# Optimization experiments

Measured on AMD Instinct MI355X. Metric: run time of the kernel, lower is better.

Reference implementation:

```python
import jax, jax.numpy as jnp
import numpy as np

EMB, HID, VOC, NLAYERS, TLEN = 256, 512, 32000, 2, 64
SRC_LEN, BS = 128, 64
DEC_HID = 2 * HID  # decoder hidden = hidden_dim * 2


def _p(key, shape, scale=0.05):
    return jax.random.normal(key, shape, dtype=jnp.float32) * scale


def setup_inputs() -> dict:
    key = jax.random.key(0)
    ks = jax.random.split(key, 24)
    d = {}
    d["sentences"] = jax.random.randint(ks[0], (SRC_LEN, BS), 0, VOC)
    d["targets"] = jax.random.randint(ks[1], (TLEN, BS), 0, VOC)
    d["emb"] = _p(ks[2], (VOC, EMB))
    # encoder: bidirectional, 2 layers; gate order i,f,g,o (PyTorch)
    d["enc0_Wih"] = _p(ks[3], (2, 4 * HID, EMB))
    d["enc0_Whh"] = _p(ks[4], (2, 4 * HID, HID))
    d["enc0_bih"] = _p(ks[5], (2, 4 * HID))
    d["enc0_bhh"] = _p(ks[6], (2, 4 * HID))
    d["enc1_Wih"] = _p(ks[7], (2, 4 * HID, 2 * HID))
    d["enc1_Whh"] = _p(ks[8], (2, 4 * HID, HID))
    d["enc1_bih"] = _p(ks[9], (2, 4 * HID))
    d["enc1_bhh"] = _p(ks[10], (2, 4 * HID))
    # decoder: unidirectional, 2 layers, hidden DEC_HID
    d["dec0_Wih"] = _p(ks[11], (4 * DEC_HID, EMB))
    d["dec0_Whh"] = _p(ks[12], (4 * DEC_HID, DEC_HID))
    d["dec0_bih"] = _p(ks[13], (4 * DEC_HID,))
    d["dec0_bhh"] = _p(ks[14], (4 * DEC_HID,))
    d["dec1_Wih"] = _p(ks[15], (4 * DEC_HID, DEC_HID))
    d["dec1_Whh"] = _p(ks[16], (4 * DEC_HID, DEC_HID))
    d["dec1_bih"] = _p(ks[17], (4 * DEC_HID,))
    d["dec1_bhh"] = _p(ks[18], (4 * DEC_HID,))
    d["W_out"] = _p(ks[19], (VOC, DEC_HID))
    d["b_out"] = _p(ks[20], (VOC,))
    return d


def lstm_scan(x, h0, c0, Wih, Whh, bih, bhh, reverse=False):
    # x: (T,B,In). Precompute input projection for the whole sequence.
    xw = jnp.einsum('tbi,gi->tbg', x, Wih) + bih  # (T,B,4H)

    def step(carry, g_in):
        h, c = carry
        g = g_in + h @ Whh.T + bhh
        i, f, gg, o = jnp.split(g, 4, axis=-1)
        c = jax.nn.sigmoid(f) * c + jax.nn.sigmoid(i) * jnp.tanh(gg)
        h = jax.nn.sigmoid(o) * jnp.tanh(c)
        return (h, c), h

    (hT, cT), ys = jax.lax.scan(step, (h0, c0), xw, reverse=reverse)
    return ys, hT, cT


def _forward(sentences, targets, emb,
             enc0_Wih, enc0_Whh, enc0_bih, enc0_bhh,
             enc1_Wih, enc1_Whh, enc1_bih, enc1_bhh,
             dec0_Wih, dec0_Whh, dec0_bih, dec0_bhh,
             dec1_Wih, dec1_Whh, dec1_bih, dec1_bhh,
             W_out, b_out):
    bs = sentences.shape[1]
    x = emb[sentences]  # (S,B,E)
    z = jnp.zeros((bs, HID), jnp.float32)
    enc_layers = ((enc0_Wih, enc0_Whh, enc0_bih, enc0_bhh),
                  (enc1_Wih, enc1_Whh, enc1_bih, enc1_bhh))
    hs, cs = [], []
    for Wih, Whh, bih, bhh in enc_layers:
        yf, hf, cf = lstm_scan(x, z, z, Wih[0], Whh[0], bih[0], bhh[0])
        yb, hb, cb = lstm_scan(x, z, z, Wih[1], Whh[1], bih[1], bhh[1], reverse=True)
        x = jnp.concatenate([yf, yb], axis=-1)  # (S,B,2H)
        hs.append(jnp.concatenate([hf, hb], axis=-1))  # _reshape_hidden concat
        cs.append(jnp.concatenate([cf, cb], axis=-1))
    # teacher forcing: decoder inputs are last source token, then targets[:-1]
    dec_tokens = jnp.concatenate([sentences[-1:], targets[:-1]], axis=0)  # (T,B)
    y = emb[dec_tokens]  # (T,B,E); dropout is identity in eval mode
    dec_layers = ((dec0_Wih, dec0_Whh, dec0_bih, dec0_bhh),
                  (dec1_Wih, dec1_Whh, dec1_bih, dec1_bhh))
    for l, (Wih, Whh, bih, bhh) in enumerate(dec_layers):
        y, _, _ = lstm_scan(y, hs[l], cs[l], Wih, Whh, bih, bhh)
    logits = jnp.einsum('tbh,vh->tbv', y, W_out) + b_out  # (T,B,V)
    return jax.nn.log_softmax(logits, axis=-1)


def reference(sentences, targets, emb,
              enc0_Wih, enc0_Whh, enc0_bih, enc0_bhh,
              enc1_Wih, enc1_Whh, enc1_bih, enc1_bhh,
              dec0_Wih, dec0_Whh, dec0_bih, dec0_bhh,
              dec1_Wih, dec1_Whh, dec1_bih, dec1_bhh,
              W_out, b_out):
    return _forward(sentences, targets, emb,
                    enc0_Wih, enc0_Whh, enc0_bih, enc0_bhh,
                    enc1_Wih, enc1_Whh, enc1_bih, enc1_bhh,
                    dec0_Wih, dec0_Whh, dec0_bih, dec0_bhh,
                    dec1_Wih, dec1_Whh, dec1_bih, dec1_bhh,
                    W_out, b_out)
```

## Files before the change

kernel.cpp:

```cpp
#include <hip/hip_runtime.h>

#define S_LEN 128
#define T_LEN 64
#define BSZ   64
#define EMBD  256
#define HID_  512
#define DHID_ 1024
#define VOC_  32000
#define HSTR  1024

typedef float  f4_t  __attribute__((ext_vector_type(4)));
typedef float  f32x4 __attribute__((ext_vector_type(4)));
typedef short  s16x8 __attribute__((ext_vector_type(8)));
typedef __bf16 bf16x8 __attribute__((ext_vector_type(8)));
typedef unsigned short u16x4 __attribute__((ext_vector_type(4)));
typedef int    i32x2 __attribute__((ext_vector_type(2)));

#define WS_XWA  0ull
#define WS_XWB  (WS_XWA + 16777216ull)
#define WS_CS   (WS_XWB + 16777216ull)
#define WS_BAR  (WS_CS  + 131072ull)
#define WS_BF   (WS_BAR + 32768ull)
#define U_X0B   0ull
#define U_HE0   (U_X0B + 2097152ull)
#define U_HE1   (U_HE0 + 8388608ull)
#define U_HD0   (U_HE1 + 8388608ull)
#define U_HD1   (U_HD0 + 4194304ull)
#define U_HSB   (U_HD1 + 4194304ull)
#define U_E0W   (U_HSB + 131072ull)
#define U_E1W   (U_E0W + 1048576ull)
#define U_D0W   (U_E1W + 4194304ull)
#define U_D1W   (U_D0W + 1048576ull)

__device__ __forceinline__ unsigned short f2bf(float x) {
    unsigned u = __builtin_bit_cast(unsigned, x);
    return (unsigned short)((u + 0x7fffu + ((u >> 16) & 1u)) >> 16);
}

__device__ __forceinline__ f4_t sc_load4(const void* p) {
    f4_t v;
    asm volatile("global_load_dwordx4 %0, %1, off sc0 sc1" : "=v"(v) : "v"(p));
    return v;
}
__device__ __forceinline__ int sc_load1(const int* p) {
    int v;
    asm volatile("global_load_dword %0, %1, off sc0 sc1\n\ts_waitcnt vmcnt(0)"
                 : "=v"(v) : "v"(p) : "memory");
    return v;
}
__device__ __forceinline__ void sc_store_int(int* p, int v) {
    asm volatile("global_store_dword %0, %1, off sc0 sc1" :: "v"(p), "v"(v) : "memory");
}
__device__ __forceinline__ void sc_store8(void* p, i32x2 v) {
    asm volatile("global_store_dwordx2 %0, %1, off sc0 sc1" :: "v"(p), "v"(v) : "memory");
}
__device__ __forceinline__ float g_load1(const float* p) {
    float v;
    asm volatile("global_load_dword %0, %1, off" : "=v"(v) : "v"(p));
    return v;
}
__device__ __forceinline__ void wait_vm0() {
    asm volatile("s_waitcnt vmcnt(0)" ::: "memory");
}
__device__ __forceinline__ void wait_vm8() {
    asm volatile("s_waitcnt vmcnt(8)" ::: "memory");
}

__device__ __forceinline__ void gload_lds16(const void* g, void* l) {
    __builtin_amdgcn_global_load_lds(
        (const __attribute__((address_space(1))) void*)g,
        (__attribute__((address_space(3))) void*)l, 16, 0, 0);
}

__device__ __forceinline__ float sigmoidf_(float x) { return 1.f / (1.f + expf(-x)); }

__global__ __launch_bounds__(256) void f2b_kernel(
    const float* __restrict__ in, unsigned short* __restrict__ out, int n4)
{
    const int stride = gridDim.x * 256;
    for (int i = blockIdx.x * 256 + threadIdx.x; i < n4; i += stride) {
        const float4 v = reinterpret_cast<const float4*>(in)[i];
        u16x4 o = { f2bf(v.x), f2bf(v.y), f2bf(v.z), f2bf(v.w) };
        reinterpret_cast<u16x4*>(out)[i] = o;
    }
}

__global__ __launch_bounds__(64) void embed_src_kernel(
    const int* __restrict__ toks, const float* __restrict__ emb,
    unsigned short* __restrict__ out)
{
    const int i = blockIdx.x;
    const int tok = toks[i];
    const float4 v = reinterpret_cast<const float4*>(emb + (size_t)tok * EMBD)[threadIdx.x];
    u16x4 o = { f2bf(v.x), f2bf(v.y), f2bf(v.z), f2bf(v.w) };
    reinterpret_cast<u16x4*>(out + (size_t)i * EMBD)[threadIdx.x] = o;
}

__global__ __launch_bounds__(64) void embed_dec_kernel(
    const int* __restrict__ sent, const int* __restrict__ targ,
    const float* __restrict__ emb, unsigned short* __restrict__ out)
{
    const int i = blockIdx.x;
    const int t = i >> 6, b = i & 63;
    const int tok = (t == 0) ? sent[(S_LEN - 1) * BSZ + b] : targ[(t - 1) * BSZ + b];
    const float4 v = reinterpret_cast<const float4*>(emb + (size_t)tok * EMBD)[threadIdx.x];
    u16x4 o = { f2bf(v.x), f2bf(v.y), f2bf(v.z), f2bf(v.w) };
    reinterpret_cast<u16x4*>(out + (size_t)i * EMBD)[threadIdx.x] = o;
}

__global__ __launch_bounds__(256) void gemm_bf16_kernel(
    const unsigned short* __restrict__ A, const unsigned short* __restrict__ B,
    const float* __restrict__ b1, const float* __restrict__ b2,
    float* __restrict__ C, int M, int N, int K, int nTN, int tmode)
{
    __shared__ __align__(16) unsigned short As[128 * 64];
    __shared__ __align__(16) unsigned short Bs[128 * 64];

    const int tid  = threadIdx.x;
    const int lane = tid & 63;
    const int wv   = tid >> 6;
    const int wm   = wv >> 1, wn = wv & 1;

    const int nwg = gridDim.x;
    const int q = nwg >> 3, r = nwg & 7;
    const int xcd = blockIdx.x & 7, io = blockIdx.x >> 3;
    const int wg = (xcd < r ? xcd * (q + 1) : r * (q + 1) + (xcd - r) * q) + io;
    const int bm = (wg / nTN) * 128;
    const int bn = (wg % nTN) * 128;

    f32x4 acc[4][4];
#pragma unroll
    for (int i = 0; i < 4; ++i)
#pragma unroll
        for (int j = 0; j < 4; ++j) acc[i][j] = (f32x4)0.f;

    const int lin_base = wv * 1024 + lane * 16;

    for (int k0 = 0; k0 < K; k0 += 64) {
        __syncthreads();
#pragma unroll
        for (int qc = 0; qc < 4; ++qc) {
            const int lin = qc * 4096 + lin_base;
            const int row = lin >> 7;
            const int c   = (lin >> 4) & 7;
            const int sc  = c ^ (row & 7);
            const size_t gofs  = (size_t)(bm + row) * K + k0 + sc * 8;
            const size_t gofsB = (size_t)(bn + row) * K + k0 + sc * 8;
            char* ldst  = (char*)As + qc * 4096 + wv * 1024;
            char* ldstB = (char*)Bs + qc * 4096 + wv * 1024;
            gload_lds16(A + gofs, ldst);
            gload_lds16(B + gofsB, ldstB);
        }
        asm volatile("s_waitcnt vmcnt(0)" ::: "memory");
        __syncthreads();
#pragma unroll
        for (int ks = 0; ks < 2; ++ks) {
            bf16x8 af[4], bfv[4];
            const int ca = ks * 4 + (lane >> 4);
#pragma unroll
            for (int f = 0; f < 4; ++f) {
                const int ra = wm * 64 + f * 16 + (lane & 15);
                af[f] = __builtin_bit_cast(bf16x8,
                    *(const s16x8*)((const char*)As + ra * 128 + ((ca ^ (ra & 7)) << 4)));
                const int rb = wn * 64 + f * 16 + (lane & 15);
                bfv[f] = __builtin_bit_cast(bf16x8,
                    *(const s16x8*)((const char*)Bs + rb * 128 + ((ca ^ (rb & 7)) << 4)));
            }
#pragma unroll
            for (int i = 0; i < 4; ++i)
#pragma unroll
                for (int j = 0; j < 4; ++j)
                    acc[i][j] = __builtin_amdgcn_mfma_f32_16x16x32_bf16(
                        af[i], bfv[j], acc[i][j], 0, 0, 0);
        }
    }

    const int col0 = bn + wn * 64 + (lane & 15);
    if (tmode == 0) {
        const int row0 = bm + wm * 64 + ((lane >> 4) << 2);
#pragma unroll
        for (int i = 0; i < 4; ++i) {
#pragma unroll
            for (int j = 0; j < 4; ++j) {
                const int col = col0 + j * 16;
                float bias = b1[col];
                if (b2) bias += b2[col];
#pragma unroll
                for (int rg = 0; rg < 4; ++rg)
                    C[(size_t)(row0 + i * 16 + rg) * N + col] = acc[i][j][rg] + bias;
            }
        }
    } else {
        const int tblk = (bm >> 6) + wm;
        const int rb = (lane >> 4) << 2;
#pragma unroll
        for (int i = 0; i < 4; ++i) {
#pragma unroll
            for (int j = 0; j < 4; ++j) {
                const int col = col0 + j * 16;
                float bias = b1[col];
                if (b2) bias += b2[col];
                float4 v = { acc[i][j][0] + bias, acc[i][j][1] + bias,
                             acc[i][j][2] + bias, acc[i][j][3] + bias };
                *reinterpret_cast<float4*>(&C[((size_t)tblk * N + col) * 64 + rb + i * 16]) = v;
            }
        }
    }
}

template<int H_T>
__global__ __launch_bounds__(256, 1) void lstm_mfma_scan(
    const float* __restrict__ xw0, const float* __restrict__ xw1,
    const float* __restrict__ Whh0, const float* __restrict__ Whh1,
    const unsigned short* __restrict__ h0b, const float* __restrict__ c0,
    unsigned short* __restrict__ hist,
    unsigned short* __restrict__ hsb, float* __restrict__ csd,
    int T, int ndir, int rev_mask, int* bar)
{
    constexpr int KST = H_T / 32;
    constexpr int CH  = H_T / 8;
    constexpr int NB  = CH / 32;

    __shared__ __align__(16) unsigned short h_lds[64 * H_T];
    __shared__ float pre[64][17];
    __shared__ __align__(8) unsigned short hpack[64][4];

    const int tid  = threadIdx.x;
    const int lane = tid & 63;
    const int w    = tid >> 6;
    const int bpd  = (ndir == 2) ? 128 : 256;
    const int dir  = blockIdx.x / bpd;
    const int blk  = blockIdx.x - dir * bpd;
    const int m0   = blk * 4;
    const int rev  = (rev_mask >> dir) & 1;
    const float* xw  = dir ? xw1  : xw0;
    const float* Whh = dir ? Whh1 : Whh0;
    const int dcol = dir * H_T;
    const int b = tid & 63;
    const int j = tid >> 6;

    int* myflag = bar + blockIdx.x * 32;
    const int* pollflag = bar + (dir * bpd + (tid < bpd ? tid : 0)) * 32;
    const bool polls = (tid < bpd);

    const int n  = lane & 15;
    const int kg = lane >> 4;
    const int wr = (n >> 2) * H_T + m0 + (n & 3);
    s16x8 wfr[KST];
#pragma unroll
    for (int ks = 0; ks < KST; ++ks) {
        const float* wp = Whh + (size_t)wr * H_T + ks * 32 + kg * 8;
        const float4 lo = *reinterpret_cast<const float4*>(wp);
        const float4 hi = *reinterpret_cast<const float4*>(wp + 4);
        s16x8 rr;
        rr[0] = (short)f2bf(lo.x); rr[1] = (short)f2bf(lo.y);
        rr[2] = (short)f2bf(lo.z); rr[3] = (short)f2bf(lo.w);
        rr[4] = (short)f2bf(hi.x); rr[5] = (short)f2bf(hi.y);
        rr[6] = (short)f2bf(hi.z); rr[7] = (short)f2bf(hi.w);
        wfr[ks] = rr;
    }

    float c  = c0 ? c0[(size_t)b * HSTR + dcol + m0 + j] : 0.f;
    float hn = 0.f;
    const int rA = w * 16 + n;
    const int rAx = rA & 7;

    for (int s = 0; s < T; ++s) {
        const int tt = rev ? (T - 1 - s) : s;

        const float* xb = xw + ((size_t)tt * (4 * H_T) + m0 + j) * 64 + b;
        float xg0 = g_load1(xb);
        float xg1 = g_load1(xb + (size_t)H_T * 64);
        float xg2 = g_load1(xb + (size_t)2 * H_T * 64);
        float xg3 = g_load1(xb + (size_t)3 * H_T * 64);

        if (s > 0) {
            int ok = polls ? 0 : 1;
            for (;;) {
                if (!ok) ok = (sc_load1(pollflag) >= s) ? 1 : 0;
                if (__syncthreads_and(ok)) break;
            }
        }

        const unsigned short* hb;
        size_t tofs;
        if (s == 0) { hb = h0b; tofs = 0; }
        else {
            const int tp = rev ? (tt + 1) : (tt - 1);
            hb = hist; tofs = (size_t)tp * (64 * 1024);
        }

        float p0 = 0.f, p1 = 0.f, p2 = 0.f, p3 = 0.f;
        if (hb) {
            f4_t bufA[8], bufB[8];
            auto issue = [&](f4_t (&bf)[8], int bt) {
#pragma unroll
                for (int jj = 0; jj < 8; ++jj) {
                    const int idx = (bt * 8 + jj) * 256 + tid;
                    const int rr_ = idx / CH, cc_ = idx % CH;
                    bf[jj] = sc_load4(hb + tofs + (size_t)rr_ * 1024 + dcol + cc_ * 8);
                }
            };
            auto writeb = [&](const f4_t (&bf)[8], int bt) {
#pragma unroll
                for (int jj = 0; jj < 8; ++jj) {
                    const int idx = (bt * 8 + jj) * 256 + tid;
                    const int rr_ = idx / CH, cc_ = idx % CH;
                    const int off = rr_ * (2 * H_T) + ((cc_ ^ (rr_ & 7)) << 4);
                    *(f4_t*)((char*)h_lds + off) = bf[jj];
                }
            };
            issue(bufA, 0);
            if (NB > 1) issue(bufB, 1);
#pragma unroll
            for (int bt = 0; bt < NB; ++bt) {
                if (bt + 1 < NB) wait_vm8(); else wait_vm0();
                if (bt & 1) writeb(bufB, bt); else writeb(bufA, bt);
                if (bt + 2 < NB) { if (bt & 1) issue(bufB, bt + 2); else issue(bufA, bt + 2); }
            }
            __syncthreads();

            f32x4 acc = {0.f, 0.f, 0.f, 0.f};
#pragma unroll
            for (int ks = 0; ks < KST; ++ks) {
                const int cc_ = ks * 4 + kg;
                const int off = rA * (2 * H_T) + ((cc_ ^ rAx) << 4);
                const bf16x8 a = __builtin_bit_cast(bf16x8,
                    *(const s16x8*)((const char*)h_lds + off));
                acc = __builtin_amdgcn_mfma_f32_16x16x32_bf16(
                    a, __builtin_bit_cast(bf16x8, wfr[ks]), acc, 0, 0, 0);
            }
            __syncthreads();
#pragma unroll
            for (int rg = 0; rg < 4; ++rg)
                pre[w * 16 + kg * 4 + rg][n] = acc[rg];
            __syncthreads();
            p0 = pre[b][0 + j]; p1 = pre[b][4 + j];
            p2 = pre[b][8 + j]; p3 = pre[b][12 + j];
        }

        asm volatile("s_waitcnt vmcnt(0)"
                     : "+v"(xg0), "+v"(xg1), "+v"(xg2), "+v"(xg3) :: "memory");

        const float ig = sigmoidf_(p0 + xg0);
        const float fg = sigmoidf_(p1 + xg1);
        const float gg = tanhf(p2 + xg2);
        const float og = sigmoidf_(p3 + xg3);
        c  = fg * c + ig * gg;
        hn = og * tanhf(c);

        hpack[b][j] = f2bf(hn);
        __syncthreads();
        if (tid < 64) {
            const i32x2 v2 = *reinterpret_cast<const i32x2*>(&hpack[tid][0]);
            sc_store8(hist + (size_t)tt * (64 * 1024) + (size_t)tid * 1024 + dcol + m0, v2);
        }
        wait_vm0();
        __syncthreads();
        if (s + 1 < T && tid == 0) sc_store_int(myflag, s + 1);
    }

    if (hsb) hsb[(size_t)b * 1024 + dcol + m0 + j] = f2bf(hn);
    if (csd) csd[(size_t)b * HSTR + dcol + m0 + j] = c;
}

__global__ __launch_bounds__(256) void logsoftmax_kernel(float* __restrict__ x, int n4)
{
    const int tid = threadIdx.x;
    float4* p = reinterpret_cast<float4*>(x + (size_t)blockIdx.x * (n4 * 4));
    float m = -3.0e38f, s = 0.f;
    for (int cc = tid; cc < n4; cc += 256) {
        const float4 v = p[cc];
        const float vv[4] = { v.x, v.y, v.z, v.w };
#pragma unroll
        for (int e = 0; e < 4; ++e) {
            const float z = vv[e];
            if (z > m) { s = s * expf(m - z) + 1.f; m = z; }
            else       { s += expf(z - m); }
        }
    }
    __shared__ float ms[256], ss[256];
    ms[tid] = m; ss[tid] = s;
    __syncthreads();
    for (int off = 128; off > 0; off >>= 1) {
        if (tid < off) {
            const float m2 = ms[tid + off], s2 = ss[tid + off];
            const float m1 = ms[tid],       s1 = ss[tid];
            const float M = fmaxf(m1, m2);
            ss[tid] = s1 * expf(m1 - M) + s2 * expf(m2 - M);
            ms[tid] = M;
        }
        __syncthreads();
    }
    const float ML = ms[0] + logf(ss[0]);
    for (int cc = tid; cc < n4; cc += 256) {
        float4 v = p[cc];
        v.x -= ML; v.y -= ML; v.z -= ML; v.w -= ML;
        p[cc] = v;
    }
}

extern "C" void kernel_launch(void* const* d_in, const int* in_sizes, int n_in,
                              void* d_out, int out_size, void* d_ws, size_t ws_size,
                              hipStream_t stream)
{
    const int*   sent  = (const int*)d_in[0];
    const int*   targ  = (const int*)d_in[1];
    const float* emb   = (const float*)d_in[2];
    const float* e0Wih = (const float*)d_in[3];
    const float* e0Whh = (const float*)d_in[4];
    const float* e0bih = (const float*)d_in[5];
    const float* e0bhh = (const float*)d_in[6];
    const float* e1Wih = (const float*)d_in[7];
    const float* e1Whh = (const float*)d_in[8];
    const float* e1bih = (const float*)d_in[9];
    const float* e1bhh = (const float*)d_in[10];
    const float* d0Wih = (const float*)d_in[11];
    const float* d0Whh = (const float*)d_in[12];
    const float* d0bih = (const float*)d_in[13];
    const float* d0bhh = (const float*)d_in[14];
    const float* d1Wih = (const float*)d_in[15];
    const float* d1Whh = (const float*)d_in[16];
    const float* d1bih = (const float*)d_in[17];
    const float* d1bhh = (const float*)d_in[18];
    const float* Wout  = (const float*)d_in[19];
    const float* bout  = (const float*)d_in[20];

    float* ws  = (float*)d_ws;
    float* xwA = ws + WS_XWA;
    float* xwB = ws + WS_XWB;
    float* cs  = ws + WS_CS;
    int*   bar = (int*)(ws + WS_BAR);
    unsigned short* ub    = (unsigned short*)(ws + WS_BF);
    unsigned short* x0b   = ub + U_X0B;
    unsigned short* h_e0  = ub + U_HE0;
    unsigned short* h_e1  = ub + U_HE1;
    unsigned short* h_d0  = ub + U_HD0;
    unsigned short* h_d1  = ub + U_HD1;
    unsigned short* hsb   = ub + U_HSB;
    unsigned short* e0Wb  = ub + U_E0W;
    unsigned short* e1Wb  = ub + U_E1W;
    unsigned short* d0Wb  = ub + U_D0W;
    unsigned short* d1Wb  = ub + U_D1W;
    unsigned short* Woutb = (unsigned short*)xwA;
    float* out = (float*)d_out;

    hipMemsetAsync(bar, 0, 4 * 8192 * sizeof(int), stream);

    f2b_kernel<<<256, 256, 0, stream>>>(e0Wih, e0Wb, 1048576 / 4);
    f2b_kernel<<<512, 256, 0, stream>>>(e1Wih, e1Wb, 4194304 / 4);
    f2b_kernel<<<256, 256, 0, stream>>>(d0Wih, d0Wb, 1048576 / 4);
    f2b_kernel<<<512, 256, 0, stream>>>(d1Wih, d1Wb, 4194304 / 4);

    embed_src_kernel<<<S_LEN * BSZ, 64, 0, stream>>>(sent, emb, x0b);
    gemm_bf16_kernel<<<64 * 16, 256, 0, stream>>>(x0b, e0Wb, e0bih, e0bhh, xwA,
                                                  S_LEN * BSZ, 2048, EMBD, 16, 1);
    gemm_bf16_kernel<<<64 * 16, 256, 0, stream>>>(x0b, e0Wb + 2048ull * 256,
                                                  e0bih + 2048, e0bhh + 2048, xwB,
                                                  S_LEN * BSZ, 2048, EMBD, 16, 1);
    lstm_mfma_scan<512><<<256, 256, 0, stream>>>(xwA, xwB, e0Whh, e0Whh + 2048ull * 512,
                                                 nullptr, nullptr, h_e0,
                                                 hsb, cs, S_LEN, 2, 2, bar);
    gemm_bf16_kernel<<<64 * 16, 256, 0, stream>>>(h_e0, e1Wb, e1bih, e1bhh, xwA,
                                                  S_LEN * BSZ, 2048, 2 * HID_, 16, 1);
    gemm_bf16_kernel<<<64 * 16, 256, 0, stream>>>(h_e0, e1Wb + 2048ull * 1024,
                                                  e1bih + 2048, e1bhh + 2048, xwB,
                                                  S_LEN * BSZ, 2048, 2 * HID_, 16, 1);
    lstm_mfma_scan<512><<<256, 256, 0, stream>>>(xwA, xwB, e1Whh, e1Whh + 2048ull * 512,
                                                 nullptr, nullptr, h_e1,
                                                 hsb + 65536, cs + 65536,
                                                 S_LEN, 2, 2, bar + 8192);
    embed_dec_kernel<<<T_LEN * BSZ, 64, 0, stream>>>(sent, targ, emb, x0b);
    gemm_bf16_kernel<<<32 * 32, 256, 0, stream>>>(x0b, d0Wb, d0bih, d0bhh, xwA,
                                                  T_LEN * BSZ, 4 * DHID_, EMBD, 32, 1);
    lstm_mfma_scan<1024><<<256, 256, 0, stream>>>(xwA, nullptr, d0Whh, nullptr,
                                                  hsb, cs, h_d0,
                                                  nullptr, nullptr, T_LEN, 1, 0,
                                                  bar + 2 * 8192);
    f2b_kernel<<<2048, 256, 0, stream>>>(Wout, Woutb, (VOC_ * DHID_) / 4);
    gemm_bf16_kernel<<<32 * 32, 256, 0, stream>>>(h_d0, d1Wb, d1bih, d1bhh, xwB,
                                                  T_LEN * BSZ, 4 * DHID_, DHID_, 32, 1);
    lstm_mfma_scan<1024><<<256, 256, 0, stream>>>(xwB, nullptr, d1Whh, nullptr,
                                                  hsb + 65536, cs + 65536, h_d1,
                                                  nullptr, nullptr, T_LEN, 1, 0,
                                                  bar + 3 * 8192);
    gemm_bf16_kernel<<<32 * 250, 256, 0, stream>>>(h_d1, Woutb, bout, nullptr, out,
                                                   T_LEN * BSZ, VOC_, DHID_, 250, 0);
    logsoftmax_kernel<<<T_LEN * BSZ, 256, 0, stream>>>(out, VOC_ / 4);
}
```

Baseline: 2.711 ms.

## Split LSTM scan by batch halves, keep Whh in LDS, store gate preactivations as bf16

The recurrent scan kernel is reorganized so each block handles 8 hidden cells for half the batch. This halves the per-step h history loaded into LDS and moves the recurrent weights from registers into LDS. The gate nonlinearities are computed in the MFMA lanes and combined via lane shuffles, which removes the pre-activation LDS round trip and two barriers per step. The input-projection GEMM now writes bf16 instead of fp32, halving xw traffic, and the next step's xw load is prefetched. This trades some precision in the gate pre-activations, and the barrier groups become per-batch-half sets of blocks.

```diff
diff --git a/kernel.cpp b/kernel.cpp
--- a/kernel.cpp
+++ b/kernel.cpp
@@ -16,25 +16,29 @@
 typedef unsigned short u16x4 __attribute__((ext_vector_type(4)));
 typedef int    i32x2 __attribute__((ext_vector_type(2)));
 
-#define WS_XWA  0ull
-#define WS_XWB  (WS_XWA + 16777216ull)
-#define WS_CS   (WS_XWB + 16777216ull)
-#define WS_BAR  (WS_CS  + 131072ull)
+#define WS_CS   0ull
+#define WS_BAR  (WS_CS + 131072ull)
 #define WS_BF   (WS_BAR + 32768ull)
 #define U_X0B   0ull
-#define U_HE0   (U_X0B + 2097152ull)
-#define U_HE1   (U_HE0 + 8388608ull)
-#define U_HD0   (U_HE1 + 8388608ull)
-#define U_HD1   (U_HD0 + 4194304ull)
-#define U_HSB   (U_HD1 + 4194304ull)
-#define U_E0W   (U_HSB + 131072ull)
-#define U_E1W   (U_E0W + 1048576ull)
-#define U_D0W   (U_E1W + 4194304ull)
-#define U_D1W   (U_D0W + 1048576ull)
+#define U_HE0   (U_X0B  + 2097152ull)
+#define U_HE1   (U_HE0  + 8388608ull)
+#define U_HD0   (U_HE1  + 8388608ull)
+#define U_HD1   (U_HD0  + 4194304ull)
+#define U_HSB   (U_HD1  + 4194304ull)
+#define U_E0W   (U_HSB  + 131072ull)
+#define U_E1W   (U_E0W  + 1048576ull)
+#define U_D0W   (U_E1W  + 4194304ull)
+#define U_D1W   (U_D0W  + 1048576ull)
+#define U_XWA   (U_D1W  + 4194304ull)
+#define U_XWB   (U_XWA  + 16777216ull)
+#define U_WOUT  (U_XWB  + 16777216ull)
 
 __device__ __forceinline__ unsigned short f2bf(float x) {
     unsigned u = __builtin_bit_cast(unsigned, x);
     return (unsigned short)((u + 0x7fffu + ((u >> 16) & 1u)) >> 16);
+}
+__device__ __forceinline__ float bf2f(unsigned u) {
+    return __builtin_bit_cast(float, u << 16);
 }
 
 __device__ __forceinline__ f4_t sc_load4(const void* p) {
@@ -51,12 +55,12 @@
 __device__ __forceinline__ void sc_store_int(int* p, int v) {
     asm volatile("global_store_dword %0, %1, off sc0 sc1" :: "v"(p), "v"(v) : "memory");
 }
-__device__ __forceinline__ void sc_store8(void* p, i32x2 v) {
-    asm volatile("global_store_dwordx2 %0, %1, off sc0 sc1" :: "v"(p), "v"(v) : "memory");
-}
-__device__ __forceinline__ float g_load1(const float* p) {
-    float v;
-    asm volatile("global_load_dword %0, %1, off" : "=v"(v) : "v"(p));
+__device__ __forceinline__ void sc_store_short(unsigned short* p, unsigned v) {
+    asm volatile("global_store_short %0, %1, off sc0 sc1" :: "v"(p), "v"(v) : "memory");
+}
+__device__ __forceinline__ i32x2 g_load8(const void* p) {
+    i32x2 v;
+    asm volatile("global_load_dwordx2 %0, %1, off" : "=v"(v) : "v"(p));
     return v;
 }
 __device__ __forceinline__ void wait_vm0() {
@@ -111,7 +115,7 @@
 __global__ __launch_bounds__(256) void gemm_bf16_kernel(
     const unsigned short* __restrict__ A, const unsigned short* __restrict__ B,
     const float* __restrict__ b1, const float* __restrict__ b2,
-    float* __restrict__ C, int M, int N, int K, int nTN, int tmode)
+    void* __restrict__ Cv, int M, int N, int K, int nTN, int tmode)
 {
     __shared__ __align__(16) unsigned short As[128 * 64];
     __shared__ __align__(16) unsigned short Bs[128 * 64];
@@ -177,6 +181,7 @@
 
     const int col0 = bn + wn * 64 + (lane & 15);
     if (tmode == 0) {
+        float* C = (float*)Cv;
         const int row0 = bm + wm * 64 + ((lane >> 4) << 2);
 #pragma unroll
         for (int i = 0; i < 4; ++i) {
@@ -191,6 +196,7 @@
             }
         }
     } else {
+        unsigned short* C = (unsigned short*)Cv;
         const int tblk = (bm >> 6) + wm;
         const int rb = (lane >> 4) << 2;
 #pragma unroll
@@ -200,9 +206,9 @@
                 const int col = col0 + j * 16;
                 float bias = b1[col];
                 if (b2) bias += b2[col];
-                float4 v = { acc[i][j][0] + bias, acc[i][j][1] + bias,
-                             acc[i][j][2] + bias, acc[i][j][3] + bias };
-                *reinterpret_cast<float4*>(&C[((size_t)tblk * N + col) * 64 + rb + i * 16]) = v;
+                u16x4 o = { f2bf(acc[i][j][0] + bias), f2bf(acc[i][j][1] + bias),
+                            f2bf(acc[i][j][2] + bias), f2bf(acc[i][j][3] + bias) };
+                *reinterpret_cast<u16x4*>(&C[((size_t)tblk * N + col) * 64 + rb + i * 16]) = o;
             }
         }
     }
@@ -210,7 +216,7 @@
 
 template<int H_T>
 __global__ __launch_bounds__(256, 1) void lstm_mfma_scan(
-    const float* __restrict__ xw0, const float* __restrict__ xw1,
+    const unsigned short* __restrict__ xw0, const unsigned short* __restrict__ xw1,
     const float* __restrict__ Whh0, const float* __restrict__ Whh1,
     const unsigned short* __restrict__ h0b, const float* __restrict__ c0,
     unsigned short* __restrict__ hist,
@@ -219,37 +225,44 @@
 {
     constexpr int KST = H_T / 32;
     constexpr int CH  = H_T / 8;
-    constexpr int NB  = CH / 32;
-
-    __shared__ __align__(16) unsigned short h_lds[64 * H_T];
-    __shared__ float pre[64][17];
-    __shared__ __align__(8) unsigned short hpack[64][4];
+    constexpr int CPT = CH / 8;
+    constexpr int NBH = CPT / 8;
+    constexpr int NCB = H_T / 8;
+
+    __shared__ __align__(16) unsigned short h_lds[32 * H_T];
+    __shared__ __align__(16) unsigned short w_lds[32 * H_T];
 
     const int tid  = threadIdx.x;
     const int lane = tid & 63;
     const int w    = tid >> 6;
-    const int bpd  = (ndir == 2) ? 128 : 256;
-    const int dir  = blockIdx.x / bpd;
-    const int blk  = blockIdx.x - dir * bpd;
-    const int m0   = blk * 4;
+    const int bq   = w & 1;
+    const int rh   = w >> 1;
+    const int n    = lane & 15;
+    const int kg   = lane >> 4;
+    const int g    = n >> 2;
+    const int cell = rh * 4 + (n & 3);
+
+    const int nbpd = 2 * NCB;
+    const int dir  = blockIdx.x / nbpd;
+    const int rem  = blockIdx.x - dir * nbpd;
+    const int bg   = rem / NCB;
+    const int cb   = rem - bg * NCB;
+    const int m0c  = cb * 8;
     const int rev  = (rev_mask >> dir) & 1;
-    const float* xw  = dir ? xw1  : xw0;
+    const unsigned short* xw = dir ? xw1 : xw0;
     const float* Whh = dir ? Whh1 : Whh0;
     const int dcol = dir * H_T;
-    const int b = tid & 63;
-    const int j = tid >> 6;
+    const int b0   = bg * 32;
 
     int* myflag = bar + blockIdx.x * 32;
-    const int* pollflag = bar + (dir * bpd + (tid < bpd ? tid : 0)) * 32;
-    const bool polls = (tid < bpd);
-
-    const int n  = lane & 15;
-    const int kg = lane >> 4;
-    const int wr = (n >> 2) * H_T + m0 + (n & 3);
-    s16x8 wfr[KST];
-#pragma unroll
-    for (int ks = 0; ks < KST; ++ks) {
-        const float* wp = Whh + (size_t)wr * H_T + ks * 32 + kg * 8;
+    const int* pollflag = bar +
+        ((dir * nbpd + bg * NCB) + (tid < NCB ? tid : 0)) * 32;
+    const bool polls = (tid < NCB);
+
+    for (int idx = tid; idx < 32 * CH; idx += 256) {
+        const int r_  = idx / CH, cc_ = idx - r_ * CH;
+        const int gg_ = r_ >> 3, cl_ = r_ & 7;
+        const float* wp = Whh + (size_t)(gg_ * H_T + m0c + cl_) * H_T + cc_ * 8;
         const float4 lo = *reinterpret_cast<const float4*>(wp);
         const float4 hi = *reinterpret_cast<const float4*>(wp + 4);
         s16x8 rr;
@@ -257,22 +270,34 @@
         rr[2] = (short)f2bf(lo.z); rr[3] = (short)f2bf(lo.w);
         rr[4] = (short)f2bf(hi.x); rr[5] = (short)f2bf(hi.y);
         rr[6] = (short)f2bf(hi.z); rr[7] = (short)f2bf(hi.w);
-        wfr[ks] = rr;
-    }
-
-    float c  = c0 ? c0[(size_t)b * HSTR + dcol + m0 + j] : 0.f;
-    float hn = 0.f;
-    const int rA = w * 16 + n;
+        *(s16x8*)((char*)w_lds + r_ * (2 * H_T) + ((cc_ ^ (r_ & 7)) << 4)) = rr;
+    }
+
+    float cst[4] = {0.f, 0.f, 0.f, 0.f};
+    if (g == 0 && c0) {
+#pragma unroll
+        for (int rg = 0; rg < 4; ++rg)
+            cst[rg] = c0[(size_t)(b0 + bq * 16 + kg * 4 + rg) * HSTR + dcol + m0c + cell];
+    }
+    float hnv[4];
+
+    const unsigned short* xbase =
+        xw + ((size_t)(g * H_T + m0c + cell)) * 64 + b0 + bq * 16 + kg * 4;
+    i32x2 xg;
+    auto issue_xg = [&](int ttn) {
+        xg = g_load8(xbase + (size_t)ttn * (4 * H_T) * 64);
+    };
+
+    const int rW  = g * 8 + cell;
+    const int rWx = rW & 7;
+    const int rA  = bq * 16 + n;
     const int rAx = rA & 7;
+
+    issue_xg(rev ? (T - 1) : 0);
+    __syncthreads();
 
     for (int s = 0; s < T; ++s) {
         const int tt = rev ? (T - 1 - s) : s;
-
-        const float* xb = xw + ((size_t)tt * (4 * H_T) + m0 + j) * 64 + b;
-        float xg0 = g_load1(xb);
-        float xg1 = g_load1(xb + (size_t)H_T * 64);
-        float xg2 = g_load1(xb + (size_t)2 * H_T * 64);
-        float xg3 = g_load1(xb + (size_t)3 * H_T * 64);
 
         if (s > 0) {
             int ok = polls ? 0 : 1;
@@ -290,78 +315,94 @@
             hb = hist; tofs = (size_t)tp * (64 * 1024);
         }
 
-        float p0 = 0.f, p1 = 0.f, p2 = 0.f, p3 = 0.f;
+        f32x4 acc = {0.f, 0.f, 0.f, 0.f};
         if (hb) {
-            f4_t bufA[8], bufB[8];
-            auto issue = [&](f4_t (&bf)[8], int bt) {
+            f4_t buf[2][8];
+            auto issue = [&](int bt) {
 #pragma unroll
                 for (int jj = 0; jj < 8; ++jj) {
                     const int idx = (bt * 8 + jj) * 256 + tid;
-                    const int rr_ = idx / CH, cc_ = idx % CH;
-                    bf[jj] = sc_load4(hb + tofs + (size_t)rr_ * 1024 + dcol + cc_ * 8);
+                    const int rr_ = idx / CH, cc_ = idx - (idx / CH) * CH;
+                    buf[bt & 1][jj] = sc_load4(
+                        hb + tofs + (size_t)(b0 + rr_) * 1024 + dcol + cc_ * 8);
                 }
             };
-            auto writeb = [&](const f4_t (&bf)[8], int bt) {
+            auto writeb = [&](int bt) {
 #pragma unroll
                 for (int jj = 0; jj < 8; ++jj) {
                     const int idx = (bt * 8 + jj) * 256 + tid;
-                    const int rr_ = idx / CH, cc_ = idx % CH;
-                    const int off = rr_ * (2 * H_T) + ((cc_ ^ (rr_ & 7)) << 4);
-                    *(f4_t*)((char*)h_lds + off) = bf[jj];
+                    const int rr_ = idx / CH, cc_ = idx - (idx / CH) * CH;
+                    *(f4_t*)((char*)h_lds + rr_ * (2 * H_T) + ((cc_ ^ (rr_ & 7)) << 4))
+                        = buf[bt & 1][jj];
                 }
             };
-            issue(bufA, 0);
-            if (NB > 1) issue(bufB, 1);
-#pragma unroll
-            for (int bt = 0; bt < NB; ++bt) {
-                if (bt + 1 < NB) wait_vm8(); else wait_vm0();
-                if (bt & 1) writeb(bufB, bt); else writeb(bufA, bt);
-                if (bt + 2 < NB) { if (bt & 1) issue(bufB, bt + 2); else issue(bufA, bt + 2); }
+            if (NBH == 1) {
+                issue(0); wait_vm0(); writeb(0);
+            } else {
+                issue(0); issue(1);
+                wait_vm8(); writeb(0);
+                wait_vm0(); writeb(1);
             }
             __syncthreads();
 
-            f32x4 acc = {0.f, 0.f, 0.f, 0.f};
 #pragma unroll
             for (int ks = 0; ks < KST; ++ks) {
-                const int cc_ = ks * 4 + kg;
-                const int off = rA * (2 * H_T) + ((cc_ ^ rAx) << 4);
+                const int ca = ks * 4 + kg;
                 const bf16x8 a = __builtin_bit_cast(bf16x8,
-                    *(const s16x8*)((const char*)h_lds + off));
-                acc = __builtin_amdgcn_mfma_f32_16x16x32_bf16(
-                    a, __builtin_bit_cast(bf16x8, wfr[ks]), acc, 0, 0, 0);
-            }
-            __syncthreads();
-#pragma unroll
-            for (int rg = 0; rg < 4; ++rg)
-                pre[w * 16 + kg * 4 + rg][n] = acc[rg];
-            __syncthreads();
-            p0 = pre[b][0 + j]; p1 = pre[b][4 + j];
-            p2 = pre[b][8 + j]; p3 = pre[b][12 + j];
-        }
-
-        asm volatile("s_waitcnt vmcnt(0)"
-                     : "+v"(xg0), "+v"(xg1), "+v"(xg2), "+v"(xg3) :: "memory");
-
-        const float ig = sigmoidf_(p0 + xg0);
-        const float fg = sigmoidf_(p1 + xg1);
-        const float gg = tanhf(p2 + xg2);
-        const float og = sigmoidf_(p3 + xg3);
-        c  = fg * c + ig * gg;
-        hn = og * tanhf(c);
-
-        hpack[b][j] = f2bf(hn);
-        __syncthreads();
-        if (tid < 64) {
-            const i32x2 v2 = *reinterpret_cast<const i32x2*>(&hpack[tid][0]);
-            sc_store8(hist + (size_t)tt * (64 * 1024) + (size_t)tid * 1024 + dcol + m0, v2);
+                    *(const s16x8*)((const char*)h_lds + rA * (2 * H_T) + ((ca ^ rAx) << 4)));
+                const bf16x8 bfr = __builtin_bit_cast(bf16x8,
+                    *(const s16x8*)((const char*)w_lds + rW * (2 * H_T) + ((ca ^ rWx) << 4)));
+                acc = __builtin_amdgcn_mfma_f32_16x16x32_bf16(a, bfr, acc, 0, 0, 0);
+            }
+        }
+
+        asm volatile("s_waitcnt vmcnt(0)" : "+v"(xg) :: "memory");
+        const unsigned x0u = (unsigned)xg[0], x1u = (unsigned)xg[1];
+        float xwf[4] = { bf2f(x0u & 0xffffu), bf2f(x0u >> 16),
+                         bf2f(x1u & 0xffffu), bf2f(x1u >> 16) };
+
+        const bool is2 = (g == 2);
+        const float kk = is2 ? 2.f : 1.f;
+        const float sub = is2 ? 1.f : 0.f;
+        float act[4];
+#pragma unroll
+        for (int rg = 0; rg < 4; ++rg) {
+            const float p = acc[rg] + xwf[rg];
+            act[rg] = kk * sigmoidf_(kk * p) - sub;
+        }
+        float x8[4], x4a[4], x4b[4];
+#pragma unroll
+        for (int rg = 0; rg < 4; ++rg) {
+            x8[rg]  = __shfl_xor(act[rg], 8);
+            x4a[rg] = __shfl_xor(act[rg], 4);
+            x4b[rg] = __shfl_xor(x8[rg], 4);
+        }
+        if (g == 0) {
+#pragma unroll
+            for (int rg = 0; rg < 4; ++rg) {
+                cst[rg] = x4a[rg] * cst[rg] + act[rg] * x8[rg];
+                hnv[rg] = x4b[rg] * tanhf(cst[rg]);
+                sc_store_short(hist + (size_t)tt * (64 * 1024)
+                               + (size_t)(b0 + bq * 16 + kg * 4 + rg) * 1024
+                               + dcol + m0c + cell, (unsigned)f2bf(hnv[rg]));
+            }
         }
         wait_vm0();
         __syncthreads();
-        if (s + 1 < T && tid == 0) sc_store_int(myflag, s + 1);
-    }
-
-    if (hsb) hsb[(size_t)b * 1024 + dcol + m0 + j] = f2bf(hn);
-    if (csd) csd[(size_t)b * HSTR + dcol + m0 + j] = c;
+        if (s + 1 < T) {
+            if (tid == 0) sc_store_int(myflag, s + 1);
+            issue_xg(rev ? (T - 2 - s) : (s + 1));
+        }
+    }
+
+    if (hsb && g == 0) {
+#pragma unroll
+        for (int rg = 0; rg < 4; ++rg) {
+            const int b_ = b0 + bq * 16 + kg * 4 + rg;
+            hsb[(size_t)b_ * 1024 + dcol + m0c + cell] = f2bf(hnv[rg]);
+            csd[(size_t)b_ * HSTR + dcol + m0c + cell] = cst[rg];
+        }
+    }
 }
 
 __global__ __launch_bounds__(256) void logsoftmax_kernel(float* __restrict__ x, int n4)
@@ -427,8 +468,6 @@
     const float* bout  = (const float*)d_in[20];
 
     float* ws  = (float*)d_ws;
-    float* xwA = ws + WS_XWA;
-    float* xwB = ws + WS_XWB;
     float* cs  = ws + WS_CS;
     int*   bar = (int*)(ws + WS_BAR);
     unsigned short* ub    = (unsigned short*)(ws + WS_BF);
@@ -442,7 +481,9 @@
     unsigned short* e1Wb  = ub + U_E1W;
     unsigned short* d0Wb  = ub + U_D0W;
     unsigned short* d1Wb  = ub + U_D1W;
-    unsigned short* Woutb = (unsigned short*)xwA;
+    unsigned short* xwA   = ub + U_XWA;
+    unsigned short* xwB   = ub + U_XWB;
+    unsigned short* Woutb = ub + U_WOUT;
     float* out = (float*)d_out;
 
     hipMemsetAsync(bar, 0, 4 * 8192 * sizeof(int), stream);
@@ -451,6 +492,7 @@
     f2b_kernel<<<512, 256, 0, stream>>>(e1Wih, e1Wb, 4194304 / 4);
     f2b_kernel<<<256, 256, 0, stream>>>(d0Wih, d0Wb, 1048576 / 4);
     f2b_kernel<<<512, 256, 0, stream>>>(d1Wih, d1Wb, 4194304 / 4);
+    f2b_kernel<<<2048, 256, 0, stream>>>(Wout, Woutb, (VOC_ * DHID_) / 4);
 
     embed_src_kernel<<<S_LEN * BSZ, 64, 0, stream>>>(sent, emb, x0b);
     gemm_bf16_kernel<<<64 * 16, 256, 0, stream>>>(x0b, e0Wb, e0bih, e0bhh, xwA,
@@ -477,7 +519,6 @@
                                                   hsb, cs, h_d0,
                                                   nullptr, nullptr, T_LEN, 1, 0,
                                                   bar + 2 * 8192);
-    f2b_kernel<<<2048, 256, 0, stream>>>(Wout, Woutb, (VOC_ * DHID_) / 4);
     gemm_bf16_kernel<<<32 * 32, 256, 0, stream>>>(h_d0, d1Wb, d1bih, d1bhh, xwB,
                                                   T_LEN * BSZ, 4 * DHID_, DHID_, 32, 1);
     lstm_mfma_scan<1024><<<256, 256, 0, stream>>>(xwB, nullptr, d1Whh, nullptr,
```

New measurement: 3.031 ms. +11.8%, slower.
